# Kernel optimization log

Hardware: AMD Instinct MI355X
Metric: run time of the kernel (lower is better)

Reference implementation:

```python
import jax, jax.numpy as jnp
import numpy as np

DIM = 768
NUM_HEADS = 8
SCALE = (DIM // NUM_HEADS) ** -0.5  # 96^-0.5, matches head_dim**-0.5
B, N = 8, 4096


def setup_inputs() -> dict:
    key = jax.random.key(0)
    k1, k2 = jax.random.split(key)
    x_1 = jax.random.normal(k1, (B, N, DIM), dtype=jnp.float32)
    x_2 = jax.random.normal(k2, (B, N, DIM), dtype=jnp.float32)
    return {"x_1": x_1, "x_2": x_2}


def reference(x_1, x_2):
    # q = x_1, k = v = x_2; channel-wise (transpose) attention
    # attn[b,c,d] = sum_n q[b,n,c] * k[b,n,d] * scale   -> [B, C, C]
    attn = jnp.einsum('bnc,bnd->bcd', x_1, x_2) * SCALE
    attn = jax.nn.softmax(attn, axis=-1)
    # out[b,c,n] = sum_d attn[b,c,d] * v[b,n,d]          -> [B, C, N]
    return jnp.einsum('bcd,bnd->bcn', attn, x_2)
```

## Files before the change

### kernel.cpp

```cpp
#include <hip/hip_runtime.h>
#include <stdint.h>

typedef _Float16 f16;
typedef _Float16 f16x4 __attribute__((ext_vector_type(4)));
typedef _Float16 f16x8 __attribute__((ext_vector_type(8)));
typedef float f32x4 __attribute__((ext_vector_type(4)));

#define NB 8
#define NN 4096
#define CC 768
#define SCALE_F 0.10206207261596577f

#define GLDS16(gp, lp)                                                       \
  __builtin_amdgcn_global_load_lds(                                          \
      (__attribute__((address_space(1))) void*)(gp),                         \
      (__attribute__((address_space(3))) void*)(lp), 16, 0, 0)

__global__ __launch_bounds__(256) void k_convert(
    const float* __restrict__ x1, const float* __restrict__ x2,
    f16* __restrict__ x1t, f16* __restrict__ x2t, f16* __restrict__ x2b) {
  __shared__ float tile[64][65];
  const int which = blockIdx.z >> 3;
  const int b = blockIdx.z & 7;
  const int n0 = blockIdx.x << 6;
  const int c0 = blockIdx.y << 6;
  const float* src = (which ? x2 : x1) + (size_t)b * NN * CC;
  f16* dt = (which ? x2t : x1t) + (size_t)b * CC * NN;
  const int t = threadIdx.x;
  const int rowi = t >> 4;
  const int col4 = (t & 15) << 2;
#pragma unroll
  for (int it = 0; it < 4; ++it) {
    const int r = it * 16 + rowi;
    const float4 v =
        *reinterpret_cast<const float4*>(&src[(size_t)(n0 + r) * CC + c0 + col4]);
    tile[r][col4 + 0] = v.x;
    tile[r][col4 + 1] = v.y;
    tile[r][col4 + 2] = v.z;
    tile[r][col4 + 3] = v.w;
    if (which) {
      f16x4 o = {(f16)v.x, (f16)v.y, (f16)v.z, (f16)v.w};
      *reinterpret_cast<f16x4*>(
          &x2b[(size_t)b * NN * CC + (size_t)(n0 + r) * CC + c0 + col4]) = o;
    }
  }
  __syncthreads();
  const int c = t >> 2;
  const int nb = (t & 3) << 4;
  f16x8 lo, hi;
#pragma unroll
  for (int j = 0; j < 8; ++j) lo[j] = (f16)tile[nb + j][c];
#pragma unroll
  for (int j = 0; j < 8; ++j) hi[j] = (f16)tile[nb + 8 + j][c];
  f16* o = &dt[(size_t)(c0 + c) * NN + n0 + nb];
  *reinterpret_cast<f16x8*>(o) = lo;
  *reinterpret_cast<f16x8*>(o + 8) = hi;
}

template <bool ATOMIC, int SWZ>
__global__ __launch_bounds__(512, 2) void k_gemm_bt(
    const f16* __restrict__ A, const f16* __restrict__ B,
    float* __restrict__ C, int klen, int lda, int ldb, int ldc,
    size_t sA, size_t sB, size_t sC) {
  __shared__ __align__(16) f16 As[2][256 * 64];
  __shared__ __align__(16) f16 Bs[2][256 * 64];

  const int lin = blockIdx.x;
  const int xcd = lin & 7;
  const int slot = lin >> 3;
  int bx, by, ks;
  const int b = xcd;
  if (SWZ == 1) {
    ks = slot / 9;
    const int item = slot % 9;
    bx = item % 3;
    by = item / 3;
  } else {
    ks = 0;
    by = slot % 3;
    bx = slot / 3;
  }

  const f16* Ap = A + (size_t)b * sA + (size_t)by * 256 * lda + (size_t)ks * klen;
  const f16* Bp = B + (size_t)b * sB + (size_t)bx * 256 * ldb + (size_t)ks * klen;
  float* Cp = C + (size_t)b * sC + (size_t)by * 256 * ldc + bx * 256;

  const int tid = threadIdx.x;
  const int wave = tid >> 6;
  const int lane = tid & 63;
  const int wr = wave >> 2;
  const int wn = wave & 3;

  const int srow = lane >> 3;
  const int ssw = ((lane & 7) ^ srow) * 8;
  const f16* gA = Ap + (size_t)(wave * 32 + srow) * lda + ssw;
  const f16* gB = Bp + (size_t)(wave * 32 + srow) * ldb + ssw;
  const int cb = wave * 4 * 512;

  const int mrow = lane & 15;
  const int kk = lane >> 4;
  const int asw = ((kk ^ (mrow & 7)) * 8);
  const int raofs = (wr * 128 + mrow) * 64 + asw;
  const int rbofs = (wn * 64 + mrow) * 64 + asw;

  f32x4 acc[8][4] = {};

  const int nit = klen >> 6;

#define STAGE(bufi)                                                          \
  do {                                                                       \
    _Pragma("unroll") for (int q = 0; q < 4; ++q) {                          \
      GLDS16(gA + (size_t)q * 8 * lda, &As[bufi][cb + q * 512]);             \
      GLDS16(gB + (size_t)q * 8 * ldb, &Bs[bufi][cb + q * 512]);             \
    }                                                                        \
  } while (0)

  STAGE(0);
  gA += 64; gB += 64;
  STAGE(1);

  for (int it = 0; it < nit; ++it) {
    const int buf = it & 1;
    if (it + 1 < nit)
      asm volatile("s_waitcnt vmcnt(8)" ::: "memory");
    else
      asm volatile("s_waitcnt vmcnt(0)" ::: "memory");
    __builtin_amdgcn_s_barrier();
    __builtin_amdgcn_sched_barrier(0);

    const f16* la = &As[buf][0];
    const f16* lb = &Bs[buf][0];
    f16x8 af[8], bf[4];
#pragma unroll
    for (int i = 0; i < 8; ++i)
      af[i] = *reinterpret_cast<const f16x8*>(la + raofs + i * 1024);
#pragma unroll
    for (int j = 0; j < 4; ++j)
      bf[j] = *reinterpret_cast<const f16x8*>(lb + rbofs + j * 1024);
#pragma unroll
    for (int i = 0; i < 8; ++i)
#pragma unroll
      for (int j = 0; j < 4; ++j)
        acc[i][j] = __builtin_amdgcn_mfma_f32_16x16x32_f16(af[i], bf[j],
                                                           acc[i][j], 0, 0, 0);
#pragma unroll
    for (int i = 0; i < 8; ++i)
      af[i] = *reinterpret_cast<const f16x8*>(la + ((raofs + i * 1024) ^ 32));
#pragma unroll
    for (int j = 0; j < 4; ++j)
      bf[j] = *reinterpret_cast<const f16x8*>(lb + ((rbofs + j * 1024) ^ 32));
    asm volatile("s_waitcnt lgkmcnt(0)" ::: "memory");
    __builtin_amdgcn_sched_barrier(0);
    __builtin_amdgcn_s_barrier();
    __builtin_amdgcn_sched_barrier(0);
    if (it + 2 < nit) {
      gA += 64; gB += 64;
      STAGE(buf);
    }
#pragma unroll
    for (int i = 0; i < 8; ++i)
#pragma unroll
      for (int j = 0; j < 4; ++j)
        acc[i][j] = __builtin_amdgcn_mfma_f32_16x16x32_f16(af[i], bf[j],
                                                           acc[i][j], 0, 0, 0);
  }
#undef STAGE

  const int col = lane & 15;
  const int rq = kk * 4;
#pragma unroll
  for (int i = 0; i < 8; ++i) {
    const int r0 = wr * 128 + i * 16 + rq;
#pragma unroll
    for (int j = 0; j < 4; ++j) {
      const int cidx = wn * 64 + j * 16 + col;
#pragma unroll
      for (int r = 0; r < 4; ++r) {
        const float v = acc[i][j][r];
        if (ATOMIC)
          atomicAdd(&Cp[(size_t)(r0 + r) * ldc + cidx], v);
        else
          Cp[(size_t)(r0 + r) * ldc + cidx] = v;
      }
    }
  }
}

__global__ __launch_bounds__(256) void k_softmax(const float* __restrict__ S,
                                                 f16* __restrict__ P) {
  const int row = blockIdx.x * 4 + (threadIdx.x >> 6);
  const int lane = threadIdx.x & 63;
  const float* s = S + (size_t)row * CC;
  float v[12];
#pragma unroll
  for (int j = 0; j < 3; ++j) {
    const float4 t = *reinterpret_cast<const float4*>(&s[j * 256 + lane * 4]);
    v[j * 4 + 0] = t.x * SCALE_F;
    v[j * 4 + 1] = t.y * SCALE_F;
    v[j * 4 + 2] = t.z * SCALE_F;
    v[j * 4 + 3] = t.w * SCALE_F;
  }
  float m = v[0];
#pragma unroll
  for (int j = 1; j < 12; ++j) m = fmaxf(m, v[j]);
#pragma unroll
  for (int off = 32; off >= 1; off >>= 1) m = fmaxf(m, __shfl_xor(m, off, 64));
  float sum = 0.f;
#pragma unroll
  for (int j = 0; j < 12; ++j) {
    v[j] = __expf(v[j] - m);
    sum += v[j];
  }
#pragma unroll
  for (int off = 32; off >= 1; off >>= 1) sum += __shfl_xor(sum, off, 64);
  const float inv = 1.0f / sum;
  f16* p = P + (size_t)row * CC;
#pragma unroll
  for (int j = 0; j < 3; ++j) {
    f16x4 o = {(f16)(v[j * 4 + 0] * inv), (f16)(v[j * 4 + 1] * inv),
               (f16)(v[j * 4 + 2] * inv), (f16)(v[j * 4 + 3] * inv)};
    *reinterpret_cast<f16x4*>(&p[j * 256 + lane * 4]) = o;
  }
}

extern "C" void kernel_launch(void* const* d_in, const int* in_sizes, int n_in,
                              void* d_out, int out_size, void* d_ws,
                              size_t ws_size, hipStream_t stream) {
  const float* x1 = (const float*)d_in[0];
  const float* x2 = (const float*)d_in[1];
  float* out = (float*)d_out;

  const size_t elems = (size_t)NB * NN * CC;
  f16* x1t = (f16*)d_out;
  f16* x2t = x1t + elems;
  char* ws = (char*)d_ws;
  f16* x2b = (f16*)ws;
  float* S = (float*)(ws + elems * 2);
  f16* P = (f16*)(ws + elems * 2 + (size_t)NB * CC * CC * 4);
  const size_t need =
      elems * 2 + (size_t)NB * CC * CC * 4 + (size_t)NB * CC * CC * 2;
  if (ws_size < need) return;

  k_convert<<<dim3(NN / 64, CC / 64, 2 * NB), 256, 0, stream>>>(x1, x2, x1t,
                                                                x2t, x2b);
  hipMemsetAsync(S, 0, (size_t)NB * CC * CC * 4, stream);
  k_gemm_bt<true, 1><<<dim3(9 * NB * 2), 512, 0, stream>>>(
      x1t, x2t, S, NN / 2, NN, NN, CC, (size_t)CC * NN, (size_t)CC * NN,
      (size_t)CC * CC);
  k_softmax<<<dim3(NB * CC / 4), 256, 0, stream>>>(S, P);
  k_gemm_bt<false, 2><<<dim3(16 * 3 * NB), 512, 0, stream>>>(
      P, x2b, out, CC, CC, CC, NN, (size_t)CC * CC, (size_t)NN * CC,
      (size_t)CC * NN);
}
```

Baseline: 412.2 us.

## Split first GEMM K into three chunks and swizzle transpose tile

The first GEMM's split-K goes from 2 to 3 chunks of 1344, with the last chunk taking 64 extra, so 216 workgroups run instead of 144 on a 256-CU part. This should fill more CUs, at the cost of more atomic traffic into S. The convert kernel's LDS tile drops the padded 65-column layout for an XOR-swizzled 64-column one. Rows are now written as float4, and each thread reads one column across 16 rows and writes 16 contiguous halves.

New measurement: 413.3 us. Within noise of the previous version (+0.3%).

```diff
diff --git a/kernel.cpp b/kernel.cpp
--- a/kernel.cpp
+++ b/kernel.cpp
@@ -19,7 +19,7 @@
 __global__ __launch_bounds__(256) void k_convert(
     const float* __restrict__ x1, const float* __restrict__ x2,
     f16* __restrict__ x1t, f16* __restrict__ x2t, f16* __restrict__ x2b) {
-  __shared__ float tile[64][65];
+  __shared__ __align__(16) float tile[64 * 64];
   const int which = blockIdx.z >> 3;
   const int b = blockIdx.z & 7;
   const int n0 = blockIdx.x << 6;
@@ -28,16 +28,16 @@
   f16* dt = (which ? x2t : x1t) + (size_t)b * CC * NN;
   const int t = threadIdx.x;
   const int rowi = t >> 4;
-  const int col4 = (t & 15) << 2;
+  const int chnk = t & 15;
+  const int col4 = chnk << 2;
+  const int swc4 = (chnk ^ rowi) << 2;
 #pragma unroll
   for (int it = 0; it < 4; ++it) {
     const int r = it * 16 + rowi;
     const float4 v =
         *reinterpret_cast<const float4*>(&src[(size_t)(n0 + r) * CC + c0 + col4]);
-    tile[r][col4 + 0] = v.x;
-    tile[r][col4 + 1] = v.y;
-    tile[r][col4 + 2] = v.z;
-    tile[r][col4 + 3] = v.w;
+    *reinterpret_cast<float4*>(&tile[r * 64 + swc4]) =
+        v;
     if (which) {
       f16x4 o = {(f16)v.x, (f16)v.y, (f16)v.z, (f16)v.w};
       *reinterpret_cast<f16x4*>(
@@ -45,16 +45,17 @@
     }
   }
   __syncthreads();
-  const int c = t >> 2;
-  const int nb = (t & 3) << 4;
-  f16x8 lo, hi;
-#pragma unroll
-  for (int j = 0; j < 8; ++j) lo[j] = (f16)tile[nb + j][c];
-#pragma unroll
-  for (int j = 0; j < 8; ++j) hi[j] = (f16)tile[nb + 8 + j][c];
-  f16* o = &dt[(size_t)(c0 + c) * NN + n0 + nb];
-  *reinterpret_cast<f16x8*>(o) = lo;
-  *reinterpret_cast<f16x8*>(o + 8) = hi;
+  const int c = t & 63;
+  const int w = t >> 6;
+  f16 ob[16];
+#pragma unroll
+  for (int j = 0; j < 16; ++j) {
+    const int n = w * 16 + j;
+    ob[j] = (f16)tile[n * 64 + (((c >> 2) ^ j) << 2) + (c & 3)];
+  }
+  f16* o = &dt[(size_t)(c0 + c) * NN + n0 + w * 16];
+  *reinterpret_cast<f16x8*>(o) = *reinterpret_cast<f16x8*>(&ob[0]);
+  *reinterpret_cast<f16x8*>(o + 8) = *reinterpret_cast<f16x8*>(&ob[8]);
 }
 
 template <bool ATOMIC, int SWZ>
@@ -81,8 +82,12 @@
     bx = slot / 3;
   }
 
-  const f16* Ap = A + (size_t)b * sA + (size_t)by * 256 * lda + (size_t)ks * klen;
-  const f16* Bp = B + (size_t)b * sB + (size_t)bx * 256 * ldb + (size_t)ks * klen;
+  const size_t kofs = (size_t)ks * klen;
+  int kl = klen;
+  if (SWZ == 1 && ks == 2) kl += 64;
+
+  const f16* Ap = A + (size_t)b * sA + (size_t)by * 256 * lda + kofs;
+  const f16* Bp = B + (size_t)b * sB + (size_t)bx * 256 * ldb + kofs;
   float* Cp = C + (size_t)b * sC + (size_t)by * 256 * ldc + bx * 256;
 
   const int tid = threadIdx.x;
@@ -105,7 +110,7 @@
 
   f32x4 acc[8][4] = {};
 
-  const int nit = klen >> 6;
+  const int nit = kl >> 6;
 
 #define STAGE(bufi)                                                          \
   do {                                                                       \
@@ -244,8 +249,8 @@
   k_convert<<<dim3(NN / 64, CC / 64, 2 * NB), 256, 0, stream>>>(x1, x2, x1t,
                                                                 x2t, x2b);
   hipMemsetAsync(S, 0, (size_t)NB * CC * CC * 4, stream);
-  k_gemm_bt<true, 1><<<dim3(9 * NB * 2), 512, 0, stream>>>(
-      x1t, x2t, S, NN / 2, NN, NN, CC, (size_t)CC * NN, (size_t)CC * NN,
+  k_gemm_bt<true, 1><<<dim3(9 * NB * 3), 512, 0, stream>>>(
+      x1t, x2t, S, 1344, NN, NN, CC, (size_t)CC * NN, (size_t)CC * NN,
       (size_t)CC * CC);
   k_softmax<<<dim3(NB * CC / 4), 256, 0, stream>>>(S, P);
   k_gemm_bt<false, 2><<<dim3(16 * 3 * NB), 512, 0, stream>>>(
```

## Fuse fp32-to-fp16 conversion and transpose into GEMM loaders, drop atomics

Applied to the files above, without the earlier changes.

Removes the separate convert/transpose kernel: both GEMMs now read fp32 inputs directly through registers, convert to fp16 and write swizzled tiles into LDS, prefetching the next tile during compute. The first GEMM uses a 3-way split-K that writes separate partial buffers, and the softmax sums them, replacing the memset and atomic adds. This avoids writing and re-reading about 150MB of fp16 copies, but the register-staged loads replace the asynchronous global-to-LDS copies and raise register pressure.

After: 344.1 us. -16.5%, faster.

```diff
diff --git a/kernel.cpp b/kernel.cpp
--- a/kernel.cpp
+++ b/kernel.cpp
@@ -11,161 +11,260 @@
 #define CC 768
 #define SCALE_F 0.10206207261596577f
 
-#define GLDS16(gp, lp)                                                       \
-  __builtin_amdgcn_global_load_lds(                                          \
-      (__attribute__((address_space(1))) void*)(gp),                         \
-      (__attribute__((address_space(3))) void*)(lp), 16, 0, 0)
-
-__global__ __launch_bounds__(256) void k_convert(
+#define CMP(v, i) ((i) == 0 ? (v).x : (i) == 1 ? (v).y : (i) == 2 ? (v).z : (v).w)
+
+__global__ __launch_bounds__(512, 2) void k_gemm1(
     const float* __restrict__ x1, const float* __restrict__ x2,
-    f16* __restrict__ x1t, f16* __restrict__ x2t, f16* __restrict__ x2b) {
-  __shared__ float tile[64][65];
-  const int which = blockIdx.z >> 3;
-  const int b = blockIdx.z & 7;
-  const int n0 = blockIdx.x << 6;
-  const int c0 = blockIdx.y << 6;
-  const float* src = (which ? x2 : x1) + (size_t)b * NN * CC;
-  f16* dt = (which ? x2t : x1t) + (size_t)b * CC * NN;
-  const int t = threadIdx.x;
-  const int rowi = t >> 4;
-  const int col4 = (t & 15) << 2;
-#pragma unroll
-  for (int it = 0; it < 4; ++it) {
-    const int r = it * 16 + rowi;
-    const float4 v =
-        *reinterpret_cast<const float4*>(&src[(size_t)(n0 + r) * CC + c0 + col4]);
-    tile[r][col4 + 0] = v.x;
-    tile[r][col4 + 1] = v.y;
-    tile[r][col4 + 2] = v.z;
-    tile[r][col4 + 3] = v.w;
-    if (which) {
-      f16x4 o = {(f16)v.x, (f16)v.y, (f16)v.z, (f16)v.w};
-      *reinterpret_cast<f16x4*>(
-          &x2b[(size_t)b * NN * CC + (size_t)(n0 + r) * CC + c0 + col4]) = o;
-    }
-  }
-  __syncthreads();
-  const int c = t >> 2;
-  const int nb = (t & 3) << 4;
-  f16x8 lo, hi;
-#pragma unroll
-  for (int j = 0; j < 8; ++j) lo[j] = (f16)tile[nb + j][c];
-#pragma unroll
-  for (int j = 0; j < 8; ++j) hi[j] = (f16)tile[nb + 8 + j][c];
-  f16* o = &dt[(size_t)(c0 + c) * NN + n0 + nb];
-  *reinterpret_cast<f16x8*>(o) = lo;
-  *reinterpret_cast<f16x8*>(o + 8) = hi;
-}
-
-template <bool ATOMIC, int SWZ>
-__global__ __launch_bounds__(512, 2) void k_gemm_bt(
-    const f16* __restrict__ A, const f16* __restrict__ B,
-    float* __restrict__ C, int klen, int lda, int ldb, int ldc,
-    size_t sA, size_t sB, size_t sC) {
+    float* __restrict__ Sp) {
   __shared__ __align__(16) f16 As[2][256 * 64];
   __shared__ __align__(16) f16 Bs[2][256 * 64];
 
   const int lin = blockIdx.x;
-  const int xcd = lin & 7;
+  const int b = lin & 7;
   const int slot = lin >> 3;
-  int bx, by, ks;
-  const int b = xcd;
-  if (SWZ == 1) {
-    ks = slot / 9;
-    const int item = slot % 9;
-    bx = item % 3;
-    by = item / 3;
-  } else {
-    ks = 0;
-    by = slot % 3;
-    bx = slot / 3;
-  }
-
-  const f16* Ap = A + (size_t)b * sA + (size_t)by * 256 * lda + (size_t)ks * klen;
-  const f16* Bp = B + (size_t)b * sB + (size_t)bx * 256 * ldb + (size_t)ks * klen;
-  float* Cp = C + (size_t)b * sC + (size_t)by * 256 * ldc + bx * 256;
+  const int ks = slot / 9;
+  const int item = slot % 9;
+  const int bx = item % 3, by = item / 3;
+  const int k0 = ks * 1344;
+  const int nit = (ks == 2) ? 22 : 21;
 
   const int tid = threadIdx.x;
-  const int wave = tid >> 6;
-  const int lane = tid & 63;
-  const int wr = wave >> 2;
-  const int wn = wave & 3;
-
-  const int srow = lane >> 3;
-  const int ssw = ((lane & 7) ^ srow) * 8;
-  const f16* gA = Ap + (size_t)(wave * 32 + srow) * lda + ssw;
-  const f16* gB = Bp + (size_t)(wave * 32 + srow) * ldb + ssw;
-  const int cb = wave * 4 * 512;
-
-  const int mrow = lane & 15;
-  const int kk = lane >> 4;
-  const int asw = ((kk ^ (mrow & 7)) * 8);
+  const int wave = tid >> 6, lane = tid & 63;
+
+  const int nq = lane & 7;
+  const int cq = wave * 8 + (lane >> 3);
+  const float* gA =
+      x1 + (size_t)b * NN * CC + (size_t)(k0 + nq * 8) * CC + by * 256 + cq * 4;
+  const float* gB =
+      x2 + (size_t)b * NN * CC + (size_t)(k0 + nq * 8) * CC + bx * 256 + cq * 4;
+  int wofs[4];
+#pragma unroll
+  for (int i = 0; i < 4; ++i) {
+    const int c = cq * 4 + i;
+    wofs[i] = c * 64 + ((nq ^ (c & 7)) << 3);
+  }
+
+  const int wr = wave >> 2, wn = wave & 3;
+  const int mrow = lane & 15, kk = lane >> 4;
+  const int asw = (kk ^ (mrow & 7)) << 3;
   const int raofs = (wr * 128 + mrow) * 64 + asw;
   const int rbofs = (wn * 64 + mrow) * 64 + asw;
 
   f32x4 acc[8][4] = {};
-
-  const int nit = klen >> 6;
-
-#define STAGE(bufi)                                                          \
+  float4 la[8], lb[8];
+
+#define G1LOAD()                                                             \
   do {                                                                       \
-    _Pragma("unroll") for (int q = 0; q < 4; ++q) {                          \
-      GLDS16(gA + (size_t)q * 8 * lda, &As[bufi][cb + q * 512]);             \
-      GLDS16(gB + (size_t)q * 8 * ldb, &Bs[bufi][cb + q * 512]);             \
+    _Pragma("unroll") for (int j = 0; j < 8; ++j) {                          \
+      la[j] = *reinterpret_cast<const float4*>(&gA[(size_t)j * CC]);         \
+      lb[j] = *reinterpret_cast<const float4*>(&gB[(size_t)j * CC]);         \
+    }                                                                        \
+    gA += (size_t)64 * CC;                                                   \
+    gB += (size_t)64 * CC;                                                   \
+  } while (0)
+
+#define G1WRITE(bufi)                                                        \
+  do {                                                                       \
+    _Pragma("unroll") for (int i = 0; i < 4; ++i) {                          \
+      f16x8 ha, hb;                                                          \
+      _Pragma("unroll") for (int j = 0; j < 8; ++j) {                        \
+        ha[j] = (f16)CMP(la[j], i);                                          \
+        hb[j] = (f16)CMP(lb[j], i);                                          \
+      }                                                                      \
+      *reinterpret_cast<f16x8*>(&As[bufi][wofs[i]]) = ha;                    \
+      *reinterpret_cast<f16x8*>(&Bs[bufi][wofs[i]]) = hb;                    \
     }                                                                        \
   } while (0)
 
-  STAGE(0);
-  gA += 64; gB += 64;
-  STAGE(1);
+  G1LOAD();
+  G1WRITE(0);
+  G1LOAD();
 
   for (int it = 0; it < nit; ++it) {
-    const int buf = it & 1;
-    if (it + 1 < nit)
-      asm volatile("s_waitcnt vmcnt(8)" ::: "memory");
-    else
-      asm volatile("s_waitcnt vmcnt(0)" ::: "memory");
+    const int cur = it & 1, nxt = cur ^ 1;
+    asm volatile("s_waitcnt lgkmcnt(0)" ::: "memory");
     __builtin_amdgcn_s_barrier();
     __builtin_amdgcn_sched_barrier(0);
-
-    const f16* la = &As[buf][0];
-    const f16* lb = &Bs[buf][0];
-    f16x8 af[8], bf[4];
-#pragma unroll
-    for (int i = 0; i < 8; ++i)
-      af[i] = *reinterpret_cast<const f16x8*>(la + raofs + i * 1024);
+    const f16* pa = &As[cur][0];
+    const f16* pb = &Bs[cur][0];
+    f16x8 af[4], bf[4];
 #pragma unroll
     for (int j = 0; j < 4; ++j)
-      bf[j] = *reinterpret_cast<const f16x8*>(lb + rbofs + j * 1024);
-#pragma unroll
-    for (int i = 0; i < 8; ++i)
-#pragma unroll
-      for (int j = 0; j < 4; ++j)
-        acc[i][j] = __builtin_amdgcn_mfma_f32_16x16x32_f16(af[i], bf[j],
-                                                           acc[i][j], 0, 0, 0);
-#pragma unroll
-    for (int i = 0; i < 8; ++i)
-      af[i] = *reinterpret_cast<const f16x8*>(la + ((raofs + i * 1024) ^ 32));
+      bf[j] = *reinterpret_cast<const f16x8*>(pb + rbofs + j * 1024);
+#pragma unroll
+    for (int h = 0; h < 2; ++h) {
+#pragma unroll
+      for (int i = 0; i < 4; ++i)
+        af[i] = *reinterpret_cast<const f16x8*>(pa + raofs + (h * 4 + i) * 1024);
+#pragma unroll
+      for (int i = 0; i < 4; ++i)
+#pragma unroll
+        for (int j = 0; j < 4; ++j)
+          acc[h * 4 + i][j] = __builtin_amdgcn_mfma_f32_16x16x32_f16(
+              af[i], bf[j], acc[h * 4 + i][j], 0, 0, 0);
+    }
+    if (it + 1 < nit) {
+      __builtin_amdgcn_sched_barrier(0);
+      G1WRITE(nxt);
+      if (it + 2 < nit) G1LOAD();
+      __builtin_amdgcn_sched_barrier(0);
+    }
 #pragma unroll
     for (int j = 0; j < 4; ++j)
-      bf[j] = *reinterpret_cast<const f16x8*>(lb + ((rbofs + j * 1024) ^ 32));
+      bf[j] = *reinterpret_cast<const f16x8*>(pb + ((rbofs + j * 1024) ^ 32));
+#pragma unroll
+    for (int h = 0; h < 2; ++h) {
+#pragma unroll
+      for (int i = 0; i < 4; ++i)
+        af[i] = *reinterpret_cast<const f16x8*>(
+            pa + ((raofs + (h * 4 + i) * 1024) ^ 32));
+#pragma unroll
+      for (int i = 0; i < 4; ++i)
+#pragma unroll
+        for (int j = 0; j < 4; ++j)
+          acc[h * 4 + i][j] = __builtin_amdgcn_mfma_f32_16x16x32_f16(
+              af[i], bf[j], acc[h * 4 + i][j], 0, 0, 0);
+    }
+  }
+#undef G1LOAD
+#undef G1WRITE
+
+  float* Cp = Sp + (size_t)ks * NB * CC * CC + (size_t)b * CC * CC +
+              (size_t)by * 256 * CC + bx * 256;
+  const int col = lane & 15;
+  const int rq = kk * 4;
+#pragma unroll
+  for (int i = 0; i < 8; ++i) {
+    const int r0 = wr * 128 + i * 16 + rq;
+#pragma unroll
+    for (int j = 0; j < 4; ++j) {
+      const int cidx = wn * 64 + j * 16 + col;
+#pragma unroll
+      for (int r = 0; r < 4; ++r)
+        Cp[(size_t)(r0 + r) * CC + cidx] = acc[i][j][r];
+    }
+  }
+}
+
+__global__ __launch_bounds__(512, 2) void k_gemm2(
+    const f16* __restrict__ P, const float* __restrict__ x2,
+    float* __restrict__ out) {
+  __shared__ __align__(16) f16 As[2][256 * 64];
+  __shared__ __align__(16) f16 Bs[2][256 * 64];
+
+  const int lin = blockIdx.x;
+  const int b = lin & 7;
+  const int slot = lin >> 3;
+  const int by = slot % 3;
+  const int bx = slot / 3;
+  const int nit = 12;
+
+  const int tid = threadIdx.x;
+  const int wave = tid >> 6, lane = tid & 63;
+
+  const int ak = tid & 7;
+  const int ar = tid >> 3;
+  const f16* gP =
+      P + (size_t)b * CC * CC + (size_t)(by * 256 + ar) * CC + ak * 8;
+  int wofsa[4];
+#pragma unroll
+  for (int i = 0; i < 4; ++i)
+    wofsa[i] = (i * 64 + ar) * 64 + ((ak ^ (ar & 7)) << 3);
+
+  const int bk = tid & 15;
+  const int br = tid >> 4;
+  const float* gB =
+      x2 + (size_t)b * NN * CC + (size_t)(bx * 256 + br) * CC + bk * 4;
+  int wofsb[8];
+#pragma unroll
+  for (int q = 0; q < 8; ++q)
+    wofsb[q] =
+        (q * 32 + br) * 64 + (((bk >> 1) ^ (br & 7)) << 3) + ((bk & 1) << 2);
+
+  const int wr = wave >> 2, wn = wave & 3;
+  const int mrow = lane & 15, kk = lane >> 4;
+  const int asw = (kk ^ (mrow & 7)) << 3;
+  const int raofs = (wr * 128 + mrow) * 64 + asw;
+  const int rbofs = (wn * 64 + mrow) * 64 + asw;
+
+  f32x4 acc[8][4] = {};
+  f16x8 lpa[4];
+  float4 lb[8];
+
+#define G2LOAD()                                                             \
+  do {                                                                       \
+    _Pragma("unroll") for (int i = 0; i < 4; ++i) lpa[i] =                   \
+        *reinterpret_cast<const f16x8*>(&gP[(size_t)(i * 64) * CC]);         \
+    _Pragma("unroll") for (int q = 0; q < 8; ++q) lb[q] =                    \
+        *reinterpret_cast<const float4*>(&gB[(size_t)(q * 32) * CC]);        \
+    gP += 64;                                                                \
+    gB += 64;                                                                \
+  } while (0)
+
+#define G2WRITE(bufi)                                                        \
+  do {                                                                       \
+    _Pragma("unroll") for (int i = 0; i < 4; ++i)                            \
+        *reinterpret_cast<f16x8*>(&As[bufi][wofsa[i]]) = lpa[i];             \
+    _Pragma("unroll") for (int q = 0; q < 8; ++q) {                          \
+      f16x4 h = {(f16)lb[q].x, (f16)lb[q].y, (f16)lb[q].z, (f16)lb[q].w};    \
+      *reinterpret_cast<f16x4*>(&Bs[bufi][wofsb[q]]) = h;                    \
+    }                                                                        \
+  } while (0)
+
+  G2LOAD();
+  G2WRITE(0);
+  G2LOAD();
+
+  for (int it = 0; it < nit; ++it) {
+    const int cur = it & 1, nxt = cur ^ 1;
     asm volatile("s_waitcnt lgkmcnt(0)" ::: "memory");
-    __builtin_amdgcn_sched_barrier(0);
     __builtin_amdgcn_s_barrier();
     __builtin_amdgcn_sched_barrier(0);
-    if (it + 2 < nit) {
-      gA += 64; gB += 64;
-      STAGE(buf);
-    }
-#pragma unroll
-    for (int i = 0; i < 8; ++i)
-#pragma unroll
-      for (int j = 0; j < 4; ++j)
-        acc[i][j] = __builtin_amdgcn_mfma_f32_16x16x32_f16(af[i], bf[j],
-                                                           acc[i][j], 0, 0, 0);
-  }
-#undef STAGE
-
+    const f16* pa = &As[cur][0];
+    const f16* pb = &Bs[cur][0];
+    f16x8 af[4], bf[4];
+#pragma unroll
+    for (int j = 0; j < 4; ++j)
+      bf[j] = *reinterpret_cast<const f16x8*>(pb + rbofs + j * 1024);
+#pragma unroll
+    for (int h = 0; h < 2; ++h) {
+#pragma unroll
+      for (int i = 0; i < 4; ++i)
+        af[i] = *reinterpret_cast<const f16x8*>(pa + raofs + (h * 4 + i) * 1024);
+#pragma unroll
+      for (int i = 0; i < 4; ++i)
+#pragma unroll
+        for (int j = 0; j < 4; ++j)
+          acc[h * 4 + i][j] = __builtin_amdgcn_mfma_f32_16x16x32_f16(
+              af[i], bf[j], acc[h * 4 + i][j], 0, 0, 0);
+    }
+    if (it + 1 < nit) {
+      __builtin_amdgcn_sched_barrier(0);
+      G2WRITE(nxt);
+      if (it + 2 < nit) G2LOAD();
+      __builtin_amdgcn_sched_barrier(0);
+    }
+#pragma unroll
+    for (int j = 0; j < 4; ++j)
+      bf[j] = *reinterpret_cast<const f16x8*>(pb + ((rbofs + j * 1024) ^ 32));
+#pragma unroll
+    for (int h = 0; h < 2; ++h) {
+#pragma unroll
+      for (int i = 0; i < 4; ++i)
+        af[i] = *reinterpret_cast<const f16x8*>(
+            pa + ((raofs + (h * 4 + i) * 1024) ^ 32));
+#pragma unroll
+      for (int i = 0; i < 4; ++i)
+#pragma unroll
+        for (int j = 0; j < 4; ++j)
+          acc[h * 4 + i][j] = __builtin_amdgcn_mfma_f32_16x16x32_f16(
+              af[i], bf[j], acc[h * 4 + i][j], 0, 0, 0);
+    }
+  }
+#undef G2LOAD
+#undef G2WRITE
+
+  float* Cp = out + (size_t)b * CC * NN + (size_t)by * 256 * NN + bx * 256;
   const int col = lane & 15;
   const int rq = kk * 4;
 #pragma unroll
@@ -175,30 +274,29 @@
     for (int j = 0; j < 4; ++j) {
       const int cidx = wn * 64 + j * 16 + col;
 #pragma unroll
-      for (int r = 0; r < 4; ++r) {
-        const float v = acc[i][j][r];
-        if (ATOMIC)
-          atomicAdd(&Cp[(size_t)(r0 + r) * ldc + cidx], v);
-        else
-          Cp[(size_t)(r0 + r) * ldc + cidx] = v;
-      }
+      for (int r = 0; r < 4; ++r)
+        Cp[(size_t)(r0 + r) * NN + cidx] = acc[i][j][r];
     }
   }
 }
 
 __global__ __launch_bounds__(256) void k_softmax(const float* __restrict__ S,
-                                                 f16* __restrict__ P) {
+                                                 f16* __restrict__ Pm) {
+  const size_t PS = (size_t)NB * CC * CC;
   const int row = blockIdx.x * 4 + (threadIdx.x >> 6);
   const int lane = threadIdx.x & 63;
-  const float* s = S + (size_t)row * CC;
+  const float* s0 = S + (size_t)row * CC;
   float v[12];
 #pragma unroll
   for (int j = 0; j < 3; ++j) {
-    const float4 t = *reinterpret_cast<const float4*>(&s[j * 256 + lane * 4]);
-    v[j * 4 + 0] = t.x * SCALE_F;
-    v[j * 4 + 1] = t.y * SCALE_F;
-    v[j * 4 + 2] = t.z * SCALE_F;
-    v[j * 4 + 3] = t.w * SCALE_F;
+    const int o = j * 256 + lane * 4;
+    const float4 t0 = *reinterpret_cast<const float4*>(&s0[o]);
+    const float4 t1 = *reinterpret_cast<const float4*>(&s0[o + PS]);
+    const float4 t2 = *reinterpret_cast<const float4*>(&s0[o + 2 * PS]);
+    v[j * 4 + 0] = (t0.x + t1.x + t2.x) * SCALE_F;
+    v[j * 4 + 1] = (t0.y + t1.y + t2.y) * SCALE_F;
+    v[j * 4 + 2] = (t0.z + t1.z + t2.z) * SCALE_F;
+    v[j * 4 + 3] = (t0.w + t1.w + t2.w) * SCALE_F;
   }
   float m = v[0];
 #pragma unroll
@@ -214,7 +312,7 @@
 #pragma unroll
   for (int off = 32; off >= 1; off >>= 1) sum += __shfl_xor(sum, off, 64);
   const float inv = 1.0f / sum;
-  f16* p = P + (size_t)row * CC;
+  f16* p = Pm + (size_t)row * CC;
 #pragma unroll
   for (int j = 0; j < 3; ++j) {
     f16x4 o = {(f16)(v[j * 4 + 0] * inv), (f16)(v[j * 4 + 1] * inv),
@@ -230,25 +328,14 @@
   const float* x2 = (const float*)d_in[1];
   float* out = (float*)d_out;
 
-  const size_t elems = (size_t)NB * NN * CC;
-  f16* x1t = (f16*)d_out;
-  f16* x2t = x1t + elems;
+  const size_t PS = (size_t)NB * CC * CC;
   char* ws = (char*)d_ws;
-  f16* x2b = (f16*)ws;
-  float* S = (float*)(ws + elems * 2);
-  f16* P = (f16*)(ws + elems * 2 + (size_t)NB * CC * CC * 4);
-  const size_t need =
-      elems * 2 + (size_t)NB * CC * CC * 4 + (size_t)NB * CC * CC * 2;
+  float* S = (float*)ws;
+  f16* P = (f16*)(ws + 3 * PS * 4);
+  const size_t need = 3 * PS * 4 + PS * 2;
   if (ws_size < need) return;
 
-  k_convert<<<dim3(NN / 64, CC / 64, 2 * NB), 256, 0, stream>>>(x1, x2, x1t,
-                                                                x2t, x2b);
-  hipMemsetAsync(S, 0, (size_t)NB * CC * CC * 4, stream);
-  k_gemm_bt<true, 1><<<dim3(9 * NB * 2), 512, 0, stream>>>(
-      x1t, x2t, S, NN / 2, NN, NN, CC, (size_t)CC * NN, (size_t)CC * NN,
-      (size_t)CC * CC);
+  k_gemm1<<<dim3(9 * 3 * NB), 512, 0, stream>>>(x1, x2, S);
   k_softmax<<<dim3(NB * CC / 4), 256, 0, stream>>>(S, P);
-  k_gemm_bt<false, 2><<<dim3(16 * 3 * NB), 512, 0, stream>>>(
-      P, x2b, out, CC, CC, CC, NN, (size_t)CC * CC, (size_t)NN * CC,
-      (size_t)CC * NN);
+  k_gemm2<<<dim3(16 * 3 * NB), 512, 0, stream>>>(P, x2, out);
 }
```
